# Kernel optimization log

Hardware: AMD Instinct MI355X
Metric: run time of the kernel (lower is better)

Reference implementation:

```python
import jax, jax.numpy as jnp
import numpy as np

DIM = 768; HEADS = 12; HEAD_DIM = 64; WIN = 14; AC = 192; R = 32; S = 1.0
SCALE = HEAD_DIM ** -0.5
EPS = 1e-5  # torch nn.LayerNorm default


def _ln(x, w, b):
    mu = x.mean(-1, keepdims=True)
    var = ((x - mu) ** 2).mean(-1, keepdims=True)
    return (x - mu) * jax.lax.rsqrt(var + EPS) * w + b


def _rel(rel_pos, n):
    # q_size == k_size == n, rel_pos has 2n-1 rows -> no interpolation branch
    coords = jnp.arange(n)[:, None] - jnp.arange(n)[None, :] + (n - 1)
    return rel_pos[coords]  # [n, n, HEAD_DIM]


def _window_partition(x, ws):
    B, H, W, C = x.shape
    ph = (ws - H % ws) % ws; pw = (ws - W % ws) % ws
    x = jnp.pad(x, ((0, 0), (0, ph), (0, pw), (0, 0)))
    Hp, Wp = H + ph, W + pw
    x = x.reshape(B, Hp // ws, ws, Wp // ws, ws, C).transpose(0, 1, 3, 2, 4, 5)
    return x.reshape(-1, ws, ws, C), (Hp, Wp)


def _window_unpartition(win, ws, pad_hw, hw):
    Hp, Wp = pad_hw; H, W = hw
    B = win.shape[0] // (Hp * Wp // ws // ws)
    x = win.reshape(B, Hp // ws, Wp // ws, ws, ws, -1).transpose(0, 1, 3, 2, 4, 5)
    x = x.reshape(B, Hp, Wp, -1)
    return x[:, :H, :W, :]


def _attention(xw, qkv_W, qkv_b, facu_W, facv_W, qfac_W, vfac_W, rel_h, rel_w, proj_W, proj_b):
    Bw, h, w, _ = xw.shape
    N = h * w
    qkv = xw @ qkv_W.T + qkv_b                     # [Bw, h, w, 3*DIM]
    fu = xw @ facu_W.T                              # FacTu; dropout = identity (eval)
    new_q = (fu @ qfac_W.T) @ facv_W.T              # q_FacTs -> FacTv
    new_v = (fu @ vfac_W.T) @ facv_W.T              # v_FacTs -> FacTv
    qkv = qkv.at[..., :DIM].add(new_q * S)
    qkv = qkv.at[..., 2 * DIM:].add(new_v * S)
    qkv = qkv.reshape(Bw, N, 3, HEADS, HEAD_DIM).transpose(2, 0, 3, 1, 4)
    qkv = qkv.reshape(3, Bw * HEADS, N, HEAD_DIM)
    q, k, v = qkv[0], qkv[1], qkv[2]
    attn = (q * SCALE) @ k.transpose(0, 2, 1)       # [Bw*HEADS, N, N]
    Rh = _rel(rel_h, h); Rw = _rel(rel_w, w)
    r_q = q.reshape(-1, h, w, HEAD_DIM)
    dh = jnp.einsum('bhwc,hkc->bhwk', r_q, Rh)
    dw = jnp.einsum('bhwc,wkc->bhwk', r_q, Rw)
    attn = (attn.reshape(-1, h, w, h, w) + dh[:, :, :, :, None] + dw[:, :, :, None, :]).reshape(-1, N, N)
    attn = jax.nn.softmax(attn, axis=-1)
    out = (attn @ v).reshape(Bw, HEADS, h, w, HEAD_DIM).transpose(0, 2, 3, 1, 4).reshape(Bw, h, w, DIM)
    return out @ proj_W.T + proj_b


def _adapter(x, d_size, nw, nb, dW, db, cW, cb, uW, ub):
    b, h, w, _ = x.shape
    y = _ln(x, nw, nb)
    y = y @ dW.T + db                               # [b, h, w, AC]
    y = y.reshape(b // d_size, d_size, h, w, AC).transpose(0, 4, 1, 2, 3)  # NCDHW
    y = jax.lax.conv_general_dilated(y, cW, (1, 1, 1), 'SAME',
                                     dimension_numbers=('NCDHW', 'OIDHW', 'NCDHW'))
    y = y + cb[None, :, None, None, None]
    y = y.transpose(0, 2, 3, 4, 1).reshape(b, h, w, AC)
    y = jax.nn.gelu(y, approximate=False)
    return x + (y @ uW.T + ub)


def reference(x, an1_w, an1_b, ad1_W, ad1_b, ac1_W, ac1_b, au1_W, au1_b,
              n1_w, n1_b, qkv_W, qkv_b, facu_W, facv_W, qfac_W, vfac_W,
              rel_h, rel_w, proj_W, proj_b,
              an2_w, an2_b, ad2_W, ad2_b, ac2_W, ac2_b, au2_W, au2_b,
              n2_w, n2_b, mlp_W1, mlp_b1, mlp_W2, mlp_b2, d_size):
    x = _adapter(x, d_size, an1_w, an1_b, ad1_W, ad1_b, ac1_W, ac1_b, au1_W, au1_b)
    shortcut = x
    y = _ln(x, n1_w, n1_b)
    H, W = y.shape[1], y.shape[2]
    y, pad_hw = _window_partition(y, WIN)
    y = _attention(y, qkv_W, qkv_b, facu_W, facv_W, qfac_W, vfac_W, rel_h, rel_w, proj_W, proj_b)
    y = _window_unpartition(y, WIN, pad_hw, (H, W))
    x = shortcut + y
    x = _adapter(x, d_size, an2_w, an2_b, ad2_W, ad2_b, ac2_W, ac2_b, au2_W, au2_b)
    h = _ln(x, n2_w, n2_b)
    h = jax.nn.gelu(h @ mlp_W1.T + mlp_b1, approximate=False)
    return x + (h @ mlp_W2.T + mlp_b2)


def setup_inputs() -> dict:
    key = jax.random.key(0)
    ks = iter(jax.random.split(key, 64))
    def rn(shape, scale=0.02):
        return jax.random.normal(next(ks), shape, dtype=jnp.float32) * scale
    B, D, HW = 1, 5, 64
    inp = {'x': jax.random.normal(next(ks), (B * D, HW, HW, DIM), dtype=jnp.float32)}
    for p in ('1', '2'):
        inp[f'an{p}_w'] = jnp.ones((DIM,), jnp.float32)
        inp[f'an{p}_b'] = jnp.zeros((DIM,), jnp.float32)
        inp[f'ad{p}_W'] = rn((AC, DIM)); inp[f'ad{p}_b'] = jnp.zeros((AC,), jnp.float32)
        inp[f'ac{p}_W'] = rn((AC, AC, 3, 3, 3)); inp[f'ac{p}_b'] = jnp.zeros((AC,), jnp.float32)
        inp[f'au{p}_W'] = rn((DIM, AC)); inp[f'au{p}_b'] = jnp.zeros((DIM,), jnp.float32)
    inp['n1_w'] = jnp.ones((DIM,), jnp.float32); inp['n1_b'] = jnp.zeros((DIM,), jnp.float32)
    inp['qkv_W'] = rn((3 * DIM, DIM)); inp['qkv_b'] = jnp.zeros((3 * DIM,), jnp.float32)
    inp['facu_W'] = rn((R, DIM)); inp['facv_W'] = rn((DIM, R))
    inp['qfac_W'] = rn((R, R)); inp['vfac_W'] = rn((R, R))
    inp['rel_h'] = rn((2 * WIN - 1, HEAD_DIM)); inp['rel_w'] = rn((2 * WIN - 1, HEAD_DIM))
    inp['proj_W'] = rn((DIM, DIM)); inp['proj_b'] = jnp.zeros((DIM,), jnp.float32)
    inp['n2_w'] = jnp.ones((DIM,), jnp.float32); inp['n2_b'] = jnp.zeros((DIM,), jnp.float32)
    inp['mlp_W1'] = rn((4 * DIM, DIM)); inp['mlp_b1'] = jnp.zeros((4 * DIM,), jnp.float32)
    inp['mlp_W2'] = rn((DIM, 4 * DIM)); inp['mlp_b2'] = jnp.zeros((DIM,), jnp.float32)
    inp['d_size'] = D
    return inp
```

## Files before the change

kernel.cpp:

```cpp
#include <hip/hip_runtime.h>

typedef unsigned short u16;
typedef __bf16 v8bf __attribute__((ext_vector_type(8)));
typedef unsigned short v8u __attribute__((ext_vector_type(8)));
typedef unsigned short v4u __attribute__((ext_vector_type(4)));
typedef float f32x4 __attribute__((ext_vector_type(4)));
typedef float f32x16 __attribute__((ext_vector_type(16)));
typedef float v8f __attribute__((ext_vector_type(8)));

static constexpr int DIMC = 768;
static constexpr int HEADS = 12;
static constexpr int WINS  = 14;
static constexpr int ACCH  = 192;
static constexpr int NTOK  = 196;
static constexpr int MW    = 24500;
static constexpr int MWP   = 24576;
static constexpr int MS    = 20480;

__device__ __forceinline__ float bf2f(u16 u) {
  union { unsigned int i; float f; } x; x.i = ((unsigned int)u) << 16; return x.f;
}
__device__ __forceinline__ u16 f2bf(float f) {
  union { float f; unsigned int i; } x; x.f = f;
  unsigned int r = x.i + 0x7fffu + ((x.i >> 16) & 1u);
  return (u16)(r >> 16);
}
__device__ __forceinline__ float gelu_f(float x) {
  float y = 0.79788456080286536f * (x + 0.044715f * x * x * x);
  y = fminf(fmaxf(y, -15.f), 15.f);
  const float e = __expf(2.f * y);
  const float th = 1.f - 2.f * __builtin_amdgcn_rcpf(e + 1.f);
  return 0.5f * x * (1.f + th);
}
__device__ __forceinline__ void cp16(const u16* g, u16* l) {
  __builtin_amdgcn_global_load_lds(
      (const __attribute__((address_space(1))) unsigned int*)(const void*)g,
      (__attribute__((address_space(3))) unsigned int*)(void*)l, 16, 0, 0);
}

__global__ void k_zero16(u16* p, int n) {
  int i = blockIdx.x * 256 + threadIdx.x;
  if (i < n) p[i] = 0;
}
__global__ void k_compute_U(const float* __restrict__ facu, const float* __restrict__ qfac,
                            const float* __restrict__ vfac, float* __restrict__ Uq,
                            float* __restrict__ Uv) {
  int idx = blockIdx.x * 256 + threadIdx.x;
  if (idx >= 2 * 768 * 32) return;
  const int which = idx / (768 * 32);
  const int rem = idx - which * 768 * 32;
  const int k = rem >> 5, b = rem & 31;
  const float* fac = which ? vfac : qfac;
  float s = 0.f;
  for (int a = 0; a < 32; ++a) s += facu[a * 768 + k] * fac[b * 32 + a];
  (which ? Uv : Uq)[rem] = s;
}
__global__ void k_build_wcomb(const float* __restrict__ qkvW, const float* __restrict__ Uq,
                              const float* __restrict__ Uv, const float* __restrict__ facv,
                              u16* __restrict__ Wc) {
  int idx = blockIdx.x * 256 + threadIdx.x;
  if (idx >= 2304 * 768) return;
  const int n = idx / 768, k = idx - n * 768;
  float v = qkvW[idx];
  if (n < 768) {
    float s = 0.f;
    for (int b = 0; b < 32; ++b) s += Uq[k * 32 + b] * facv[n * 32 + b];
    v += s;
  } else if (n >= 1536) {
    const int nn = n - 1536;
    float s = 0.f;
    for (int b = 0; b < 32; ++b) s += Uv[k * 32 + b] * facv[nn * 32 + b];
    v += s;
  }
  Wc[idx] = f2bf(v);
}
__global__ void k_cast_pad(const float* __restrict__ src, u16* __restrict__ dst,
                           int rows, int cols, int rowsPad) {
  int idx = blockIdx.x * 256 + threadIdx.x;
  const int base = idx * 4;
  if (base >= rowsPad * cols) return;
  const int r = base / cols;
  v4u o;
  if (r < rows) {
    const float4 v = *(const float4*)(src + base);
    o[0] = f2bf(v.x); o[1] = f2bf(v.y); o[2] = f2bf(v.z); o[3] = f2bf(v.w);
  } else {
    o[0] = o[1] = o[2] = o[3] = 0;
  }
  *(v4u*)(dst + base) = o;
}
__global__ void k_conv_repack(const float* __restrict__ src, u16* __restrict__ dst) {
  int idx = blockIdx.x * 256 + threadIdx.x;
  const int base = idx * 4;
  if (base >= 256 * 5184) return;
  const int co = base / 5184;
  const int rem = base - co * 5184;
  const int tap = rem / 192, ci = rem - tap * 192;
  v4u o;
  if (co < 192) {
    const float* sp = src + co * 5184 + ci * 27 + tap;
#pragma unroll
    for (int e = 0; e < 4; ++e) o[e] = f2bf(sp[e * 27]);
  } else {
    o[0] = o[1] = o[2] = o[3] = 0;
  }
  *(v4u*)(dst + base) = o;
}

template<bool WINDOWED>
__global__ __launch_bounds__(256)
void ln_k(const float* __restrict__ X, const float* __restrict__ w,
          const float* __restrict__ b, u16* __restrict__ out) {
  const int r = (int)blockIdx.x;
  const int t = (int)threadIdx.x;
  int src = r;
  bool zero = false;
  if (WINDOWED) {
    if (r >= MW) zero = true;
    else {
      const int win = r / NTOK, tk = r - win * NTOK;
      const int img = win / 25, wrem = win - img * 25, wy = wrem / 5, wx = wrem - wy * 5;
      const int ty = tk / WINS, tx = tk - ty * WINS;
      const int y = wy * WINS + ty, x = wx * WINS + tx;
      if (y >= 64 || x >= 64) zero = true;
      else src = (img << 12) + (y << 6) + x;
    }
  }
  u16* orow = out + (size_t)r * DIMC;
  if (zero) {
    for (int c = t; c < DIMC; c += 256) orow[c] = 0;
    return;
  }
  const float* xr = X + (size_t)src * DIMC;
  const float v0 = xr[t], v1 = xr[t + 256], v2 = xr[t + 512];
  float s = v0 + v1 + v2, ss = v0 * v0 + v1 * v1 + v2 * v2;
#pragma unroll
  for (int o = 32; o > 0; o >>= 1) { s += __shfl_xor(s, o, 64); ss += __shfl_xor(ss, o, 64); }
  __shared__ float red[8];
  const int wave = t >> 6, lane = t & 63;
  if (lane == 0) { red[wave] = s; red[4 + wave] = ss; }
  __syncthreads();
  s = red[0] + red[1] + red[2] + red[3];
  ss = red[4] + red[5] + red[6] + red[7];
  const float mean = s * (1.0f / 768.0f);
  const float var = ss * (1.0f / 768.0f) - mean * mean;
  const float rstd = rsqrtf(var + 1e-5f);
  orow[t]       = f2bf((v0 - mean) * rstd * w[t]       + b[t]);
  orow[t + 256] = f2bf((v1 - mean) * rstd * w[t + 256] + b[t + 256]);
  orow[t + 512] = f2bf((v2 - mean) * rstd * w[t + 512] + b[t + 512]);
}

template<int EPI, bool CONV, int BK>
__global__ __launch_bounds__(256)
void gemm_bt(const u16* __restrict__ A, const u16* __restrict__ B,
             const float* __restrict__ bias, const float* __restrict__ resid,
             float* __restrict__ outF, u16* __restrict__ outB,
             int M, int N, int K, const u16* __restrict__ zrow, int GN) {
  __shared__ u16 smem[2 * 128 * BK];
  u16* At = smem;
  u16* Bt = smem + 128 * BK;
  const int gx = (int)gridDim.x;
  const int nwg = gx * (int)gridDim.y;
  const int lin = (int)blockIdx.y * gx + (int)blockIdx.x;
  const int csz = nwg >> 3;
  const int xcd = lin & 7;
  const int c = lin >> 3;
  const int bmc = csz / gx;
  const int gsz = bmc * GN;
  const int grp = c / gsz, rr = c - grp * gsz;
  const int bn = grp * GN + (rr % GN);
  const int bm = xcd * bmc + (rr / GN);
  const int t = (int)threadIdx.x;
  const int wave = t >> 6, lane = t & 63;
  const int wm = wave >> 1, wn = wave & 1;
  const int li = lane & 15, lq = lane >> 4;
  const int l31 = lane & 31, lh = lane >> 5;

  f32x4 acc[4][4];
  f32x16 acc32[2][2];
  const f32x4 vzero = {0.f, 0.f, 0.f, 0.f};
  if (BK == 64) {
#pragma unroll
    for (int a = 0; a < 4; ++a)
#pragma unroll
      for (int b = 0; b < 4; ++b) acc[a][b] = vzero;
  } else {
#pragma unroll
    for (int a = 0; a < 2; ++a)
#pragma unroll
      for (int b = 0; b < 2; ++b)
#pragma unroll
        for (int e = 0; e < 16; ++e) acc32[a][b][e] = 0.f;
  }

  const int nk = K / BK;
  for (int kt = 0; kt < nk; ++kt) {
    if (BK == 64) {
      const int lrow = lane >> 3;
      const int c16s = (lane & 7) ^ lrow;
      int cD = 0, cY = 0, cX = 0, cblk = 0;
      if (CONV) {
        const int tap = kt / 3;
        cblk = (kt - tap * 3) << 6;
        const int kd = tap / 9, r9 = tap - kd * 9, ky = r9 / 3;
        cD = kd - 1; cY = ky - 1; cX = (r9 - ky * 3) - 1;
      }
#pragma unroll
      for (int i = 0; i < 4; ++i) {
        const int r0 = i * 32 + wave * 8;
        const int grow = bm * 128 + r0 + lrow;
        const u16* src;
        if (CONV) {
          const int d = (grow >> 12) + cD, y = ((grow >> 6) & 63) + cY, x = (grow & 63) + cX;
          if ((unsigned)d < 5u && (unsigned)y < 64u && (unsigned)x < 64u)
            src = A + (size_t)((d << 12) + (y << 6) + x) * ACCH + cblk + c16s * 8;
          else
            src = zrow + c16s * 8;
        } else {
          src = A + (size_t)grow * K + (kt << 6) + c16s * 8;
        }
        cp16(src, &At[r0 * 64]);
      }
#pragma unroll
      for (int i = 0; i < 4; ++i) {
        const int r0 = i * 32 + wave * 8;
        const int grow = bn * 128 + r0 + lrow;
        cp16(B + (size_t)grow * K + (kt << 6) + c16s * 8, &Bt[r0 * 64]);
      }
    } else {
      const int srow4 = lane >> 4;
      const int sc = lane & 15;
#pragma unroll
      for (int i = 0; i < 8; ++i) {
        const int rbase = i * 16 + wave * 4;
        const int row = rbase + srow4;
        const int c16s = sc ^ (row & 15);
        cp16(A + (size_t)(bm * 128 + row) * K + kt * 128 + c16s * 8, &At[rbase * 128]);
      }
#pragma unroll
      for (int i = 0; i < 8; ++i) {
        const int rbase = i * 16 + wave * 4;
        const int row = rbase + srow4;
        const int c16s = sc ^ (row & 15);
        cp16(B + (size_t)(bn * 128 + row) * K + kt * 128 + c16s * 8, &Bt[rbase * 128]);
      }
    }
    __syncthreads();
    if (BK == 64) {
#pragma unroll
      for (int kk = 0; kk < 2; ++kk) {
        v8bf af[4], bg[4];
#pragma unroll
        for (int mf = 0; mf < 4; ++mf) {
          const int row = wm * 64 + mf * 16 + li;
          const int c16 = (kk * 4 + lq) ^ (li & 7);
          af[mf] = *(const v8bf*)&At[row * 64 + c16 * 8];
        }
#pragma unroll
        for (int nf = 0; nf < 4; ++nf) {
          const int row = wn * 64 + nf * 16 + li;
          const int c16 = (kk * 4 + lq) ^ (li & 7);
          bg[nf] = *(const v8bf*)&Bt[row * 64 + c16 * 8];
        }
#pragma unroll
        for (int mf = 0; mf < 4; ++mf)
#pragma unroll
          for (int nf = 0; nf < 4; ++nf)
            acc[mf][nf] = __builtin_amdgcn_mfma_f32_16x16x32_bf16(af[mf], bg[nf], acc[mf][nf], 0, 0, 0);
      }
    } else {
#pragma unroll
      for (int kk = 0; kk < 8; ++kk) {
        const int ch = kk * 2 + lh;
        v8bf a2[2], b2[2];
#pragma unroll
        for (int mb = 0; mb < 2; ++mb) {
          const int row = wm * 64 + mb * 32 + l31;
          a2[mb] = *(const v8bf*)&At[row * 128 + (ch ^ (row & 15)) * 8];
        }
#pragma unroll
        for (int nb = 0; nb < 2; ++nb) {
          const int row = wn * 64 + nb * 32 + l31;
          b2[nb] = *(const v8bf*)&Bt[row * 128 + (ch ^ (row & 15)) * 8];
        }
#pragma unroll
        for (int mb = 0; mb < 2; ++mb)
#pragma unroll
          for (int nb = 0; nb < 2; ++nb)
            acc32[mb][nb] = __builtin_amdgcn_mfma_f32_32x32x16_bf16(a2[mb], b2[nb], acc32[mb][nb], 0, 0, 0);
      }
    }
    __syncthreads();
  }

  if (EPI == 1 || EPI == 2 || EPI == 4) {
    u16* Ct = smem;
    if (BK == 64) {
#pragma unroll
      for (int mf = 0; mf < 4; ++mf)
#pragma unroll
        for (int nf = 0; nf < 4; ++nf)
#pragma unroll
          for (int r = 0; r < 4; ++r) {
            const int row = wm * 64 + mf * 16 + lq * 4 + r;
            const int col = wn * 64 + nf * 16 + li;
            float v = acc[mf][nf][r] + bias[bn * 128 + col];
            if (EPI == 2) v = gelu_f(v);
            Ct[row * 128 + (col ^ ((row & 7) << 3))] = f2bf(v);
          }
    } else {
#pragma unroll
      for (int mb = 0; mb < 2; ++mb)
#pragma unroll
        for (int nb = 0; nb < 2; ++nb)
#pragma unroll
          for (int rg = 0; rg < 16; ++rg) {
            const int row = wm * 64 + mb * 32 + (rg & 3) + 8 * (rg >> 2) + 4 * lh;
            const int col = wn * 64 + nb * 32 + l31;
            float v = acc32[mb][nb][rg] + bias[bn * 128 + col];
            if (EPI == 2) v = gelu_f(v);
            Ct[row * 128 + (col ^ ((row & 7) << 3))] = f2bf(v);
          }
    }
    __syncthreads();
#pragma unroll
    for (int it = 0; it < 8; ++it) {
      const int row = it * 16 + (t >> 4);
      const int seg = t & 15;
      const int gr = bm * 128 + row;
      const int col8 = bn * 128 + seg * 8;
      if (gr < M && col8 < N) {
        v8u val = *(const v8u*)&Ct[row * 128 + ((seg ^ (row & 7)) * 8)];
        if (EPI == 4) {
          const int sec = col8 / 768;
          const int hm = col8 - sec * 768;
          const int hd = hm >> 6, dd = hm & 63;
          const int win = gr / 196, tk = gr - win * 196;
          *(v8u*)(outB + (size_t)(((win * HEADS + hd) * 3 + sec) * NTOK + tk) * 64 + dd) = val;
        } else {
          *(v8u*)(outB + (size_t)gr * N + col8) = val;
        }
      }
    }
  } else {
    float* Cf = (float*)smem;
#pragma unroll
    for (int h2 = 0; h2 < 2; ++h2) {
      if (h2) __syncthreads();
      if (wm == h2) {
        if (BK == 64) {
#pragma unroll
          for (int mf = 0; mf < 4; ++mf)
#pragma unroll
            for (int nf = 0; nf < 4; ++nf)
#pragma unroll
              for (int r = 0; r < 4; ++r) {
                const int row = mf * 16 + lq * 4 + r;
                const int col = wn * 64 + nf * 16 + li;
                const float v = acc[mf][nf][r] + bias[bn * 128 + col];
                Cf[row * 128 + (col ^ (((row >> 2) & 3) << 3))] = v;
              }
        } else {
#pragma unroll
          for (int mb = 0; mb < 2; ++mb)
#pragma unroll
            for (int nb = 0; nb < 2; ++nb)
#pragma unroll
              for (int rg = 0; rg < 16; ++rg) {
                const int row = mb * 32 + (rg & 3) + 8 * (rg >> 2) + 4 * lh;
                const int col = wn * 64 + nb * 32 + l31;
                const float v = acc32[mb][nb][rg] + bias[bn * 128 + col];
                Cf[row * 128 + (col ^ (((row >> 2) & 3) << 3))] = v;
              }
        }
      }
      __syncthreads();
#pragma unroll
      for (int it = 0; it < 4; ++it) {
        const int row = it * 16 + (t >> 4);
        const int seg = t & 15;
        const int gr = bm * 128 + h2 * 64 + row;
        const int col8 = bn * 128 + seg * 8;
        if (gr < M && col8 < N) {
          v8f val = *(const v8f*)&Cf[row * 128 + ((seg ^ ((row >> 2) & 3)) * 8)];
          if (EPI == 3) {
            const float* rp = resid + (size_t)gr * N + col8;
#pragma unroll
            for (int e = 0; e < 8; ++e) val[e] += rp[e];
            *(v8f*)(outF + (size_t)gr * N + col8) = val;
          } else {
            const int win = gr / 196, tk = gr - win * 196;
            const int img = win / 25, wrem = win - img * 25, wy = wrem / 5, wx = wrem - wy * 5;
            const int ty = tk / WINS, tx = tk - ty * WINS;
            const int y = wy * WINS + ty, x = wx * WINS + tx;
            if (y < 64 && x < 64) {
              const size_t o = (size_t)((img << 12) + (y << 6) + x) * DIMC + col8;
              const float* rp = resid + o;
#pragma unroll
              for (int e = 0; e < 8; ++e) val[e] += rp[e];
              *(v8f*)(outF + o) = val;
            }
          }
        }
      }
    }
  }
}

__global__ __launch_bounds__(512, 2)
void attn_k(const u16* __restrict__ qkvR, const float* __restrict__ relh,
            const float* __restrict__ relw, u16* __restrict__ out) {
  const int blk = (int)blockIdx.x;
  const int win = blk / HEADS, h = blk - win * HEADS;
  const int t = (int)threadIdx.x, w = t >> 6, lane = t & 63;
  const int li = lane & 15, g = lane >> 4;
  const int nmf = (w < 6) ? 2 : (w == 6 ? 1 : 0);

  __shared__ u16 Kt[64 * 64];
  __shared__ u16 Vt[64 * 64];
  __shared__ u16 Pb[8 * 32 * 32];
  __shared__ u16 dhwT[28 * 268];

  const u16* Qb = qkvR + (size_t)(win * HEADS + h) * 3 * NTOK * 64;
  const u16* Kb = Qb + NTOK * 64;
  const u16* Vb = Kb + NTOK * 64;

  v8bf qf[2][2];
#pragma unroll
  for (int mf = 0; mf < 2; ++mf) {
    const int row = min(32 * w + mf * 16 + li, NTOK - 1);
#pragma unroll
    for (int ks = 0; ks < 2; ++ks)
      qf[mf][ks] = *(const v8bf*)(Qb + (size_t)row * 64 + ks * 32 + g * 8);
  }

  u16* relb = Pb;
  for (int idx = t; idx < 2 * 32 * 64; idx += 512) {
    const int which = idx >> 11, rem = idx & 2047, r = rem >> 6, c = rem & 63;
    const float v = (r < 27) ? (which ? relw[r * 64 + c] : relh[r * 64 + c]) : 0.f;
    relb[which * 2048 + r * 64 + (((c >> 3) ^ (r & 7)) * 8) + (c & 7)] = f2bf(v);
  }
  __syncthreads();

  {
    f32x4 dacc[2][2], eacc[2][2];
    const f32x4 vz = {0.f, 0.f, 0.f, 0.f};
#pragma unroll
    for (int mf = 0; mf < 2; ++mf)
#pragma unroll
      for (int nf = 0; nf < 2; ++nf) { dacc[mf][nf] = vz; eacc[mf][nf] = vz; }
#pragma unroll
    for (int ks = 0; ks < 2; ++ks) {
#pragma unroll
      for (int nf = 0; nf < 2; ++nf) {
        const int row = nf * 16 + li;
        const int off = row * 64 + (((ks * 4 + g) ^ (li & 7)) * 8);
        v8bf bh = *(const v8bf*)&relb[off];
        v8bf bw = *(const v8bf*)&relb[2048 + off];
#pragma unroll
        for (int mf = 0; mf < 2; ++mf) if (mf < nmf) {
          dacc[mf][nf] = __builtin_amdgcn_mfma_f32_16x16x32_bf16(qf[mf][ks], bh, dacc[mf][nf], 0, 0, 0);
          eacc[mf][nf] = __builtin_amdgcn_mfma_f32_16x16x32_bf16(qf[mf][ks], bw, eacc[mf][nf], 0, 0, 0);
        }
      }
    }
#pragma unroll
    for (int mf = 0; mf < 2; ++mf) if (mf < nmf)
#pragma unroll
      for (int nf = 0; nf < 2; ++nf)
#pragma unroll
        for (int r = 0; r < 4; ++r) {
          const int i = 32 * w + mf * 16 + 4 * g + r;
          if (i < 196) {
            const int c = nf * 16 + li;
            const int ih = (i * 2341) >> 15, iw = i - ih * 14;
            const int jh = ih + 13 - c;
            if ((unsigned)jh < 14u) dhwT[jh * 268 + i] = f2bf(dacc[mf][nf][r]);
            const int jw = iw + 13 - c;
            if ((unsigned)jw < 14u) dhwT[(14 + jw) * 268 + i] = f2bf(eacc[mf][nf][r]);
          }
        }
  }
  __syncthreads();

  f32x4 oacc[2][4];
  const f32x4 vz = {0.f, 0.f, 0.f, 0.f};
#pragma unroll
  for (int a = 0; a < 2; ++a)
#pragma unroll
    for (int b = 0; b < 4; ++b) oacc[a][b] = vz;
  float mrun[8], lrun[8];
#pragma unroll
  for (int a = 0; a < 8; ++a) { mrun[a] = -1e30f; lrun[a] = 0.f; }

  u16* Pw = Pb + w * 1024;
  const int jv = t & 63;
  const int dv = w * 8;

  for (int jt = 0; jt < 4; ++jt) {
    const int j0 = jt * 64;
    const int njf = (jt < 3) ? 4 : 1;
    const int nhalf = (jt < 3) ? 2 : 1;

    {
      const int rbase = w * 8;
      const int row = rbase + (lane >> 3);
      const int jg = min(j0 + row, NTOK - 1);
      const int cbs = (lane & 7) ^ (row & 7);
      cp16(Kb + (size_t)jg * 64 + cbs * 8, &Kt[rbase * 64]);
    }
    __builtin_amdgcn_sched_barrier(0);
    const int jgv = min(j0 + jv, NTOK - 1);
    v8u vg = *(const v8u*)(Vb + (size_t)jgv * 64 + dv);
    __builtin_amdgcn_sched_barrier(0);
    asm volatile("s_waitcnt vmcnt(1)" ::: "memory");
    __builtin_amdgcn_sched_barrier(0);
    __builtin_amdgcn_s_barrier();
    __builtin_amdgcn_sched_barrier(0);

    f32x4 sacc[2][4];
#pragma unroll
    for (int a = 0; a < 2; ++a)
#pragma unroll
      for (int b = 0; b < 4; ++b) sacc[a][b] = vz;
    if (nmf > 0) {
#pragma unroll
      for (int ks = 0; ks < 2; ++ks) {
#pragma unroll
        for (int jf = 0; jf < 4; ++jf) if (jf < njf) {
          const int row = jf * 16 + li;
          v8bf kb = *(const v8bf*)&Kt[row * 64 + (((ks * 4 + g) ^ (li & 7)) * 8)];
#pragma unroll
          for (int mf = 0; mf < 2; ++mf) if (mf < nmf)
            sacc[mf][jf] = __builtin_amdgcn_mfma_f32_16x16x32_bf16(qf[mf][ks], kb, sacc[mf][jf], 0, 0, 0);
        }
      }
    }

    asm volatile("s_waitcnt vmcnt(0)" ::: "memory");
    __builtin_amdgcn_sched_barrier(0);
#pragma unroll
    for (int e = 0; e < 8; ++e) {
      const int da = dv + e;
      Vt[da * 64 + (((jv >> 3) ^ (da & 7)) * 8) + (jv & 7)] = vg[e];
    }

#pragma unroll
    for (int jf = 0; jf < 4; ++jf) if (jf < njf) {
      const int j = j0 + jf * 16 + li;
      const bool jok = j < 196;
      int jh = (j * 2341) >> 15;
      const int jw = j - jh * 14;
      if (jh > 13) jh = 13;
#pragma unroll
      for (int mf = 0; mf < 2; ++mf) if (mf < nmf) {
        const int i0 = 32 * w + mf * 16 + 4 * g;
        v4u hv = *(const v4u*)&dhwT[jh * 268 + i0];
        v4u wv = *(const v4u*)&dhwT[(14 + jw) * 268 + i0];
#pragma unroll
        for (int r = 0; r < 4; ++r) {
          float v;
          if (jok && (i0 + r) < 196)
            v = sacc[mf][jf][r] * 0.125f + bf2f(hv[r]) + bf2f(wv[r]);
          else v = -1e30f;
          sacc[mf][jf][r] = v;
        }
      }
    }

#pragma unroll
    for (int mf = 0; mf < 2; ++mf) if (mf < nmf)
#pragma unroll
      for (int r = 0; r < 4; ++r) {
        float tmx = -1e30f;
#pragma unroll
        for (int jf = 0; jf < 4; ++jf) if (jf < njf) tmx = fmaxf(tmx, sacc[mf][jf][r]);
#pragma unroll
        for (int o = 1; o < 16; o <<= 1) tmx = fmaxf(tmx, __shfl_xor(tmx, o, 16));
        const int idx = mf * 4 + r;
        const float mnew = fmaxf(mrun[idx], tmx);
        const float sf = __expf(mrun[idx] - mnew);
        mrun[idx] = mnew;
        float ls = 0.f;
#pragma unroll
        for (int jf = 0; jf < 4; ++jf) if (jf < njf) {
          const float p = __expf(sacc[mf][jf][r] - mnew);
          sacc[mf][jf][r] = p;
          ls += p;
        }
#pragma unroll
        for (int o = 1; o < 16; o <<= 1) ls += __shfl_xor(ls, o, 16);
        lrun[idx] = lrun[idx] * sf + ls;
#pragma unroll
        for (int nf = 0; nf < 4; ++nf) oacc[mf][nf][r] *= sf;
      }

#pragma unroll
    for (int half = 0; half < 2; ++half) if (half < nhalf) {
#pragma unroll
      for (int c = 0; c < 2; ++c) {
        const int jf = half * 2 + c;
        const int jloc = c * 16 + li;
#pragma unroll
        for (int mf = 0; mf < 2; ++mf)
#pragma unroll
          for (int r = 0; r < 4; ++r) {
            const int il = mf * 16 + 4 * g + r;
            u16 pv = 0;
            if (mf < nmf && jf < njf) pv = f2bf(sacc[mf][jf][r]);
            Pw[il * 32 + (jloc ^ (g << 3))] = pv;
          }
      }
      if (half == 0) __syncthreads();
      if (nmf > 0) {
        v8bf pa[2];
#pragma unroll
        for (int mf = 0; mf < 2; ++mf) {
          const int row = mf * 16 + li;
          pa[mf] = *(const v8bf*)&Pw[row * 32 + ((g ^ ((li >> 2) & 3)) * 8)];
        }
#pragma unroll
        for (int nf = 0; nf < 4; ++nf) {
          const int d = nf * 16 + li;
          v8bf vb = *(const v8bf*)&Vt[d * 64 + (((half * 4 + g) ^ (li & 7)) * 8)];
#pragma unroll
          for (int mf = 0; mf < 2; ++mf)
            oacc[mf][nf] = __builtin_amdgcn_mfma_f32_16x16x32_bf16(pa[mf], vb, oacc[mf][nf], 0, 0, 0);
        }
      }
    }
    __syncthreads();
  }

  if (nmf > 0) {
    float rinv[8];
#pragma unroll
    for (int a = 0; a < 8; ++a) rinv[a] = 1.0f / lrun[a];
#pragma unroll
    for (int half = 0; half < 2; ++half) {
#pragma unroll
      for (int c = 0; c < 2; ++c) {
        const int nf = half * 2 + c;
        const int dloc = c * 16 + li;
#pragma unroll
        for (int mf = 0; mf < 2; ++mf)
#pragma unroll
          for (int r = 0; r < 4; ++r) {
            const int il = mf * 16 + 4 * g + r;
            float val = (mf < nmf) ? oacc[mf][nf][r] * rinv[mf * 4 + r] : 0.f;
            Pw[il * 32 + (dloc ^ (g << 3))] = f2bf(val);
          }
      }
#pragma unroll
      for (int p = 0; p < 2; ++p) {
        const int row = p * 16 + (lane >> 2);
        const int seg = lane & 3;
        const int i = 32 * w + row;
        if (i < 196) {
          const int segp = seg ^ ((row >> 2) & 3);
          v8u val = *(const v8u*)&Pw[row * 32 + segp * 8];
          *(v8u*)(out + (size_t)(win * NTOK + i) * DIMC + h * 64 + half * 32 + seg * 8) = val;
        }
      }
    }
  }
}

extern "C" void kernel_launch(void* const* d_in, const int* in_sizes, int n_in,
                              void* d_out, int out_size, void* d_ws, size_t ws_size,
                              hipStream_t stream) {
  (void)in_sizes; (void)n_in; (void)out_size; (void)ws_size;
  const float* x0     = (const float*)d_in[0];
  const float* an1_w  = (const float*)d_in[1];
  const float* an1_b  = (const float*)d_in[2];
  const float* ad1_W  = (const float*)d_in[3];
  const float* ad1_b  = (const float*)d_in[4];
  const float* ac1_W  = (const float*)d_in[5];
  const float* ac1_b  = (const float*)d_in[6];
  const float* au1_W  = (const float*)d_in[7];
  const float* au1_b  = (const float*)d_in[8];
  const float* an2_w  = (const float*)d_in[9];
  const float* an2_b  = (const float*)d_in[10];
  const float* ad2_W  = (const float*)d_in[11];
  const float* ad2_b  = (const float*)d_in[12];
  const float* ac2_W  = (const float*)d_in[13];
  const float* ac2_b  = (const float*)d_in[14];
  const float* au2_W  = (const float*)d_in[15];
  const float* au2_b  = (const float*)d_in[16];
  const float* n1_w   = (const float*)d_in[17];
  const float* n1_b   = (const float*)d_in[18];
  const float* qkv_W  = (const float*)d_in[19];
  const float* qkv_b  = (const float*)d_in[20];
  const float* facu_W = (const float*)d_in[21];
  const float* facv_W = (const float*)d_in[22];
  const float* qfac_W = (const float*)d_in[23];
  const float* vfac_W = (const float*)d_in[24];
  const float* rel_h  = (const float*)d_in[25];
  const float* rel_w  = (const float*)d_in[26];
  const float* proj_W = (const float*)d_in[27];
  const float* proj_b = (const float*)d_in[28];
  const float* n2_w   = (const float*)d_in[29];
  const float* n2_b   = (const float*)d_in[30];
  const float* mlp_W1 = (const float*)d_in[31];
  const float* mlp_b1 = (const float*)d_in[32];
  const float* mlp_W2 = (const float*)d_in[33];
  const float* mlp_b2 = (const float*)d_in[34];

  char* ws = (char*)d_ws;
  size_t off = 0;
  auto alloc = [&](size_t bytes) -> void* {
    void* p = (void*)(ws + off);
    off += (bytes + 255) & ~(size_t)255;
    return p;
  };
  u16*  bufA  = (u16*)alloc((size_t)MS * 3072 * 2);
  u16*  bufB  = (u16*)alloc((size_t)MWP * DIMC * 2);
  float* bufX = (float*)alloc((size_t)MS * DIMC * 4);
  u16*  bufD  = (u16*)alloc((size_t)MS * ACCH * 2);
  u16*  bufE  = (u16*)alloc((size_t)MS * ACCH * 2);
  u16*  Wcomb = (u16*)alloc((size_t)2304 * 768 * 2);
  u16*  Wproj = (u16*)alloc((size_t)768 * 768 * 2);
  u16*  Wm1   = (u16*)alloc((size_t)3072 * 768 * 2);
  u16*  Wm2   = (u16*)alloc((size_t)768 * 3072 * 2);
  u16*  Wad1  = (u16*)alloc((size_t)256 * 768 * 2);
  u16*  Wau1  = (u16*)alloc((size_t)768 * 192 * 2);
  u16*  Wcv1  = (u16*)alloc((size_t)256 * 5184 * 2);
  u16*  Wad2  = (u16*)alloc((size_t)256 * 768 * 2);
  u16*  Wau2  = (u16*)alloc((size_t)768 * 192 * 2);
  u16*  Wcv2  = (u16*)alloc((size_t)256 * 5184 * 2);
  float* Uq   = (float*)alloc(768 * 32 * 4);
  float* Uv   = (float*)alloc(768 * 32 * 4);
  u16*  zrow  = (u16*)alloc(256);

  k_zero16<<<1, 256, 0, stream>>>(zrow, 128);
  k_compute_U<<<192, 256, 0, stream>>>(facu_W, qfac_W, vfac_W, Uq, Uv);
  k_build_wcomb<<<(2304 * 768 + 255) / 256, 256, 0, stream>>>(qkv_W, Uq, Uv, facv_W, Wcomb);
  k_cast_pad<<<(768 * 768 / 4 + 255) / 256, 256, 0, stream>>>(proj_W, Wproj, 768, 768, 768);
  k_cast_pad<<<(3072 * 768 / 4 + 255) / 256, 256, 0, stream>>>(mlp_W1, Wm1, 3072, 768, 3072);
  k_cast_pad<<<(768 * 3072 / 4 + 255) / 256, 256, 0, stream>>>(mlp_W2, Wm2, 768, 3072, 768);
  k_cast_pad<<<(256 * 768 / 4 + 255) / 256, 256, 0, stream>>>(ad1_W, Wad1, 192, 768, 256);
  k_cast_pad<<<(768 * 192 / 4 + 255) / 256, 256, 0, stream>>>(au1_W, Wau1, 768, 192, 768);
  k_cast_pad<<<(256 * 768 / 4 + 255) / 256, 256, 0, stream>>>(ad2_W, Wad2, 192, 768, 256);
  k_cast_pad<<<(768 * 192 / 4 + 255) / 256, 256, 0, stream>>>(au2_W, Wau2, 768, 192, 768);
  k_conv_repack<<<(256 * 5184 / 4 + 255) / 256, 256, 0, stream>>>(ac1_W, Wcv1);
  k_conv_repack<<<(256 * 5184 / 4 + 255) / 256, 256, 0, stream>>>(ac2_W, Wcv2);

  ln_k<false><<<MS, 256, 0, stream>>>(x0, an1_w, an1_b, bufB);
  gemm_bt<1, false, 128><<<dim3(2, 160), 256, 0, stream>>>(bufB, Wad1, ad1_b, nullptr, nullptr, bufD, MS, 192, 768, nullptr, 2);
  gemm_bt<2, true, 64><<<dim3(2, 160), 256, 0, stream>>>(bufD, Wcv1, ac1_b, nullptr, nullptr, bufE, MS, 192, 5184, zrow, 2);
  gemm_bt<3, false, 64><<<dim3(6, 160), 256, 0, stream>>>(bufE, Wau1, au1_b, x0, bufX, nullptr, MS, 768, 192, nullptr, 6);

  ln_k<true><<<MWP, 256, 0, stream>>>(bufX, n1_w, n1_b, bufB);
  gemm_bt<4, false, 128><<<dim3(18, 192), 256, 0, stream>>>(bufB, Wcomb, qkv_b, nullptr, nullptr, bufA, MW, 2304, 768, nullptr, 6);
  attn_k<<<125 * HEADS, 512, 0, stream>>>(bufA, rel_h, rel_w, bufB);
  gemm_bt<5, false, 128><<<dim3(6, 192), 256, 0, stream>>>(bufB, Wproj, proj_b, bufX, bufX, nullptr, MW, 768, 768, nullptr, 6);

  ln_k<false><<<MS, 256, 0, stream>>>(bufX, an2_w, an2_b, bufB);
  gemm_bt<1, false, 128><<<dim3(2, 160), 256, 0, stream>>>(bufB, Wad2, ad2_b, nullptr, nullptr, bufD, MS, 192, 768, nullptr, 2);
  gemm_bt<2, true, 64><<<dim3(2, 160), 256, 0, stream>>>(bufD, Wcv2, ac2_b, nullptr, nullptr, bufE, MS, 192, 5184, zrow, 2);
  gemm_bt<3, false, 64><<<dim3(6, 160), 256, 0, stream>>>(bufE, Wau2, au2_b, bufX, bufX, nullptr, MS, 768, 192, nullptr, 6);

  ln_k<false><<<MS, 256, 0, stream>>>(bufX, n2_w, n2_b, bufB);
  gemm_bt<2, false, 128><<<dim3(24, 160), 256, 0, stream>>>(bufB, Wm1, mlp_b1, nullptr, nullptr, bufA, MS, 3072, 768, nullptr, 8);
  gemm_bt<3, false, 128><<<dim3(6, 160), 256, 0, stream>>>(bufA, Wm2, mlp_b2, bufX, (float*)d_out, nullptr, MS, 768, 3072, nullptr, 6);
}
```

Measured before the change: 1.029 ms.

## Split each attention window-head across two 256-thread blocks by query rows

The attention kernel now launches two blocks per window-head, each with 4 waves that handle half of the query row tiles (global wave index rh*4+w). Each block still stages the full K and V tiles for every key tile, now with each thread loading twice as many rows and V columns, and computes the relative-position terms only for its own rows. The goal is more, smaller blocks and better occupancy and scheduling (launch bounds 256,3). The cost is duplicated K/V global loads and staging per window-head, plus imbalance: the second block has one partly idle wave and one fully idle wave.

```diff
diff --git a/kernel.cpp b/kernel.cpp
--- a/kernel.cpp
+++ b/kernel.cpp
@@ -407,18 +407,21 @@
   }
 }
 
-__global__ __launch_bounds__(512, 2)
+__global__ __launch_bounds__(256, 3)
 void attn_k(const u16* __restrict__ qkvR, const float* __restrict__ relh,
             const float* __restrict__ relw, u16* __restrict__ out) {
   const int blk = (int)blockIdx.x;
-  const int win = blk / HEADS, h = blk - win * HEADS;
+  const int rh = blk & 1;
+  const int wh = blk >> 1;
+  const int win = wh / HEADS, h = wh - win * HEADS;
   const int t = (int)threadIdx.x, w = t >> 6, lane = t & 63;
+  const int gw = rh * 4 + w;
   const int li = lane & 15, g = lane >> 4;
-  const int nmf = (w < 6) ? 2 : (w == 6 ? 1 : 0);
+  const int nmf = (gw < 6) ? 2 : (gw == 6 ? 1 : 0);
 
   __shared__ u16 Kt[64 * 64];
   __shared__ u16 Vt[64 * 64];
-  __shared__ u16 Pb[8 * 32 * 32];
+  __shared__ u16 Pb[4 * 32 * 32];
   __shared__ u16 dhwT[28 * 268];
 
   const u16* Qb = qkvR + (size_t)(win * HEADS + h) * 3 * NTOK * 64;
@@ -428,14 +431,14 @@
   v8bf qf[2][2];
 #pragma unroll
   for (int mf = 0; mf < 2; ++mf) {
-    const int row = min(32 * w + mf * 16 + li, NTOK - 1);
+    const int row = min(32 * gw + mf * 16 + li, NTOK - 1);
 #pragma unroll
     for (int ks = 0; ks < 2; ++ks)
       qf[mf][ks] = *(const v8bf*)(Qb + (size_t)row * 64 + ks * 32 + g * 8);
   }
 
   u16* relb = Pb;
-  for (int idx = t; idx < 2 * 32 * 64; idx += 512) {
+  for (int idx = t; idx < 2 * 32 * 64; idx += 256) {
     const int which = idx >> 11, rem = idx & 2047, r = rem >> 6, c = rem & 63;
     const float v = (r < 27) ? (which ? relw[r * 64 + c] : relh[r * 64 + c]) : 0.f;
     relb[which * 2048 + r * 64 + (((c >> 3) ^ (r & 7)) * 8) + (c & 7)] = f2bf(v);
@@ -470,7 +473,7 @@
       for (int nf = 0; nf < 2; ++nf)
 #pragma unroll
         for (int r = 0; r < 4; ++r) {
-          const int i = 32 * w + mf * 16 + 4 * g + r;
+          const int i = 32 * gw + mf * 16 + 4 * g + r;
           if (i < 196) {
             const int c = nf * 16 + li;
             const int ih = (i * 2341) >> 15, iw = i - ih * 14;
@@ -495,15 +498,16 @@
 
   u16* Pw = Pb + w * 1024;
   const int jv = t & 63;
-  const int dv = w * 8;
+  const int dv = (t >> 6) * 16;
 
   for (int jt = 0; jt < 4; ++jt) {
     const int j0 = jt * 64;
     const int njf = (jt < 3) ? 4 : 1;
     const int nhalf = (jt < 3) ? 2 : 1;
 
-    {
-      const int rbase = w * 8;
+#pragma unroll
+    for (int is = 0; is < 2; ++is) {
+      const int rbase = w * 16 + is * 8;
       const int row = rbase + (lane >> 3);
       const int jg = min(j0 + row, NTOK - 1);
       const int cbs = (lane & 7) ^ (row & 7);
@@ -511,9 +515,11 @@
     }
     __builtin_amdgcn_sched_barrier(0);
     const int jgv = min(j0 + jv, NTOK - 1);
-    v8u vg = *(const v8u*)(Vb + (size_t)jgv * 64 + dv);
+    const u16* vp = Vb + (size_t)jgv * 64 + dv;
+    v8u vg0 = *(const v8u*)vp;
+    v8u vg1 = *(const v8u*)(vp + 8);
     __builtin_amdgcn_sched_barrier(0);
-    asm volatile("s_waitcnt vmcnt(1)" ::: "memory");
+    asm volatile("s_waitcnt vmcnt(2)" ::: "memory");
     __builtin_amdgcn_sched_barrier(0);
     __builtin_amdgcn_s_barrier();
     __builtin_amdgcn_sched_barrier(0);
@@ -541,8 +547,9 @@
     __builtin_amdgcn_sched_barrier(0);
 #pragma unroll
     for (int e = 0; e < 8; ++e) {
-      const int da = dv + e;
-      Vt[da * 64 + (((jv >> 3) ^ (da & 7)) * 8) + (jv & 7)] = vg[e];
+      const int da = dv + e, db = dv + 8 + e;
+      Vt[da * 64 + (((jv >> 3) ^ (da & 7)) * 8) + (jv & 7)] = vg0[e];
+      Vt[db * 64 + (((jv >> 3) ^ (db & 7)) * 8) + (jv & 7)] = vg1[e];
     }
 
 #pragma unroll
@@ -554,7 +561,7 @@
       if (jh > 13) jh = 13;
 #pragma unroll
       for (int mf = 0; mf < 2; ++mf) if (mf < nmf) {
-        const int i0 = 32 * w + mf * 16 + 4 * g;
+        const int i0 = 32 * gw + mf * 16 + 4 * g;
         v4u hv = *(const v4u*)&dhwT[jh * 268 + i0];
         v4u wv = *(const v4u*)&dhwT[(14 + jw) * 268 + i0];
 #pragma unroll
@@ -655,7 +662,7 @@
       for (int p = 0; p < 2; ++p) {
         const int row = p * 16 + (lane >> 2);
         const int seg = lane & 3;
-        const int i = 32 * w + row;
+        const int i = 32 * gw + row;
         if (i < 196) {
           const int segp = seg ^ ((row >> 2) & 3);
           v8u val = *(const v8u*)&Pw[row * 32 + segp * 8];
@@ -752,7 +759,7 @@
 
   ln_k<true><<<MWP, 256, 0, stream>>>(bufX, n1_w, n1_b, bufB);
   gemm_bt<4, false, 128><<<dim3(18, 192), 256, 0, stream>>>(bufB, Wcomb, qkv_b, nullptr, nullptr, bufA, MW, 2304, 768, nullptr, 6);
-  attn_k<<<125 * HEADS, 512, 0, stream>>>(bufA, rel_h, rel_w, bufB);
+  attn_k<<<125 * HEADS * 2, 256, 0, stream>>>(bufA, rel_h, rel_w, bufB);
   gemm_bt<5, false, 128><<<dim3(6, 192), 256, 0, stream>>>(bufB, Wproj, proj_b, bufX, bufX, nullptr, MW, 768, 768, nullptr, 6);
 
   ln_k<false><<<MS, 256, 0, stream>>>(bufX, an2_w, an2_b, bufB);
```

After: 998.0 us. -3.0%, faster.
